# Kernel tuning notes

Measured on AMD Instinct MI355X. Metric: run time of the kernel, lower is better.

The kernel has to match this reference:

```python
import jax, jax.numpy as jnp
import numpy as np

COMMITMENT_COST = 0.25
NUM_EMBEDDINGS = 512
EMBEDDING_DIM = 128


def setup_inputs() -> dict:
    key = jax.random.key(0)
    k1, k2 = jax.random.split(key)
    z = jax.random.normal(k1, (64, 128, 32, 32), dtype=jnp.float32)
    # nn.Embedding weight initialized uniform(-1/K, 1/K)
    lim = 1.0 / NUM_EMBEDDINGS
    emb_weight = jax.random.uniform(
        k2, (NUM_EMBEDDINGS, EMBEDDING_DIM), dtype=jnp.float32,
        minval=-lim, maxval=lim)
    return {"z": z, "emb_weight": emb_weight}


def reference(z, emb_weight):
    b, c, h, w = z.shape  # c == embedding_dim
    # (b, h, w, c) -> (b*h*w, c)
    z_cl = jnp.transpose(z, (0, 2, 3, 1))
    z_flat = z_cl.reshape(b * h * w, c)
    # squared L2 distances: ||z||^2 + ||e||^2 - 2 z.e  -> [N, K]
    distances = (
        jnp.sum(z_flat ** 2, axis=-1, keepdims=True)
        + jnp.sum(emb_weight ** 2, axis=-1)[None, :]
        - 2.0 * jnp.matmul(z_flat, emb_weight.T)
    )
    encoding_indices = jnp.argmin(distances, axis=-1)  # [N]
    z_q = emb_weight[encoding_indices]                 # [N, c]
    z_q = z_q.reshape(b, h, w, c)
    z_q = jnp.transpose(z_q, (0, 3, 1, 2))             # [b, c, h, w]
    loss = (
        jnp.mean((z_q - jax.lax.stop_gradient(z)) ** 2)
        + COMMITMENT_COST * jnp.mean((jax.lax.stop_gradient(z_q) - z) ** 2)
    )
    # straight-through estimator
    z_q_st = z + jax.lax.stop_gradient(z_q - z)
    return (z_q_st, loss, encoding_indices)
```

## Files before the change

kernel.cpp:

```cpp
#include <hip/hip_runtime.h>


#define D_DIM 128
#define HW    1024
#define GAP_THR 2.5e-4f
#define FLAG_CAP 16384

typedef short short8 __attribute__((ext_vector_type(8)));
typedef float f32x16 __attribute__((ext_vector_type(16)));

union U8 { unsigned int u[4]; short8 s; uint4 q; };

__device__ __forceinline__ unsigned short f2bf(float v) {
    unsigned int u = __builtin_bit_cast(unsigned int, v);
    return (unsigned short)((u + 0x7fffu + ((u >> 16) & 1u)) >> 16);
}
__device__ __forceinline__ float bfhi(unsigned short h) {
    unsigned int u = ((unsigned int)h) << 16;
    return __builtin_bit_cast(float, u);
}
__device__ __forceinline__ unsigned int umn(unsigned int a, unsigned int b) {
    return a < b ? a : b;
}
__device__ __forceinline__ unsigned int umx(unsigned int a, unsigned int b) {
    return a > b ? a : b;
}

__global__ void prep_kernel(const float* __restrict__ emb,
                            float* __restrict__ etr,
                            uint4* __restrict__ ebh, uint4* __restrict__ ebl,
                            float* __restrict__ se) {
    const int t = blockIdx.x * 256 + threadIdx.x;

    {
        const int k = t >> 7;
        const int d = t & 127;
        etr[d * 512 + k] = emb[t];
    }

    if (t < 8192) {
        const int lane = t & 63;
        const int ks   = (t >> 6) & 7;
        const int kcol = t >> 9;
        const int krow = kcol * 32 + (lane & 31);
        const int d0   = ks * 16 + (lane >> 5) * 8;
        const float* ep = emb + (size_t)krow * D_DIM + d0;
        float v[8];
        #pragma unroll
        for (int j = 0; j < 8; ++j) v[j] = ep[j];
        U8 hh, ll;
        #pragma unroll
        for (int p = 0; p < 4; ++p) {
            const unsigned short h0 = f2bf(v[2*p]), h1 = f2bf(v[2*p+1]);
            const unsigned short l0 = f2bf(v[2*p]   - bfhi(h0));
            const unsigned short l1 = f2bf(v[2*p+1] - bfhi(h1));
            hh.u[p] = (unsigned int)h0 | ((unsigned int)h1 << 16);
            ll.u[p] = (unsigned int)l0 | ((unsigned int)l1 << 16);
        }
        ebh[t] = hh.q;
        ebl[t] = ll.q;
    }

    if (t < 512) {
        const float* e = emb + (size_t)t * D_DIM;
        float r[8];
        #pragma unroll
        for (int j = 0; j < 8; ++j) {
            float v = e[j];
            float p = v * v;
            asm("" : "+v"(p));
            r[j] = p;
        }
        for (int i = 8; i < 128; i += 8) {
            #pragma unroll
            for (int j = 0; j < 8; ++j) {
                float v = e[i + j];
                float p = v * v;
                asm("" : "+v"(p));
                r[j] += p;
            }
        }
        se[t] = ((r[0] + r[1]) + (r[2] + r[3])) + ((r[4] + r[5]) + (r[6] + r[7]));
    }
}

__launch_bounds__(256, 1)
__global__ void dist_kernel(const float* __restrict__ z,
                            const uint4* __restrict__ ebh,
                            const uint4* __restrict__ ebl,
                            const float* __restrict__ se_g,
                            const float* __restrict__ emb,
                            float* __restrict__ idx_out,
                            unsigned int* __restrict__ flag_cnt,
                            int* __restrict__ flag_list,
                            float* __restrict__ zq,
                            double* __restrict__ loss) {
    __shared__ int   li_sh[128];
    __shared__ float ept[D_DIM * 33];
    __shared__ float lred[4];

    const int tid  = threadIdx.x;
    const int lane = tid & 63;
    const int wid  = tid >> 6;
    const int row  = lane & 31;
    const int nblk = blockIdx.x * 128;
    const int bimg = nblk >> 10;
    const int hw0  = nblk & 1023;
    const int n0   = nblk + wid * 32;
    const int hww  = hw0 + wid * 32;

    short8 Ah[8], Al[8];
    {
        const float* zc = z + (size_t)bimg * (D_DIM * HW) + hww + row;
        #pragma unroll
        for (int ks = 0; ks < 8; ++ks) {
            const int d0 = ks * 16 + (lane >> 5) * 8;
            float v[8];
            #pragma unroll
            for (int j = 0; j < 8; ++j) v[j] = zc[(size_t)(d0 + j) * HW];
            U8 hh, ll;
            #pragma unroll
            for (int p = 0; p < 4; ++p) {
                unsigned int hwd, lwd;
                asm("v_cvt_pk_bf16_f32 %0, %1, %2" : "=v"(hwd) : "v"(v[2*p]), "v"(v[2*p+1]));
                const float xh = __builtin_bit_cast(float, hwd << 16);
                const float yh = __builtin_bit_cast(float, hwd & 0xffff0000u);
                const float xl = v[2*p]   - xh;
                const float yl = v[2*p+1] - yh;
                asm("v_cvt_pk_bf16_f32 %0, %1, %2" : "=v"(lwd) : "v"(xl), "v"(yl));
                hh.u[p] = hwd; ll.u[p] = lwd;
            }
            Ah[ks] = hh.s; Al[ks] = ll.s;
        }
    }

    unsigned int b1[16], b2[16];
    #pragma unroll
    for (int j = 0; j < 16; ++j) { b1[j] = 0xFFFFFFFFu; b2[j] = 0xFFFFFFFFu; }

    for (int kc = 0; kc < 16; ++kc) {
        const int   kgl  = kc * 32 + row;
        const float sevp = se_g[kgl] + 0.5f;
        const uint4* pbh = ebh + kc * 512 + lane;
        const uint4* pbl = ebl + kc * 512 + lane;

        f32x16 ahh, ahl, alh;
        #pragma unroll
        for (int j = 0; j < 16; ++j) { ahh[j] = 0.f; ahl[j] = 0.f; alh[j] = 0.f; }

        #pragma unroll
        for (int ks = 0; ks < 8; ++ks) {
            U8 bh; bh.q = pbh[ks * 64];
            U8 bl; bl.q = pbl[ks * 64];
            ahh = __builtin_amdgcn_mfma_f32_32x32x16_bf16(Ah[ks], bh.s, ahh, 0, 0, 0);
            ahl = __builtin_amdgcn_mfma_f32_32x32x16_bf16(Ah[ks], bl.s, ahl, 0, 0, 0);
            alh = __builtin_amdgcn_mfma_f32_32x32x16_bf16(Al[ks], bh.s, alh, 0, 0, 0);
        }

        #pragma unroll
        for (int j = 0; j < 16; ++j) {
            const float dot = (ahh[j] + ahl[j]) + alh[j];
            const float pd  = fmaf(-2.f, dot, sevp);
            const unsigned int key =
                (__builtin_bit_cast(unsigned int, pd) & 0xFFFFFE00u) | (unsigned int)kgl;
            const unsigned int m = umn(key, b1[j]);
            b2[j] = umn(umx(key, b1[j]), b2[j]);
            b1[j] = m;
        }
    }

    #pragma unroll
    for (int off = 1; off <= 16; off <<= 1) {
        #pragma unroll
        for (int j = 0; j < 16; ++j) {
            const unsigned int o1 = (unsigned int)__shfl_xor((int)b1[j], off);
            const unsigned int o2 = (unsigned int)__shfl_xor((int)b2[j], off);
            const unsigned int m  = umn(b1[j], o1);
            b2[j] = umn(umx(b1[j], o1), umn(b2[j], o2));
            b1[j] = m;
        }
    }

    if ((lane & 31) == 0) {
        const int half = lane >> 5;
        #pragma unroll
        for (int j = 0; j < 16; ++j) {
            const int r = (j & 3) + 8 * (j >> 2) + 4 * half;
            const int n = n0 + r;
            const int code = (int)(b1[j] & 511u);
            idx_out[n] = (float)code;
            li_sh[wid * 32 + r] = code;
            const float f1 = __builtin_bit_cast(float, b1[j] & 0xFFFFFE00u);
            const float f2 = __builtin_bit_cast(float, b2[j] & 0xFFFFFE00u);
            if (f2 - f1 < GAP_THR) {
                unsigned int p = atomicAdd(flag_cnt, 1u);
                if (p < FLAG_CAP) flag_list[p] = n;
            }
        }
    }

    float lacc = 0.f;
    for (int h = 0; h < 4; ++h) {
        __syncthreads();
        {
            const int p   = tid >> 3;
            const int sub = tid & 7;
            const float* er = emb + (size_t)li_sh[h * 32 + p] * D_DIM + sub * 16;
            #pragma unroll
            for (int j4 = 0; j4 < 4; ++j4) {
                const float4 v = *(const float4*)(er + j4 * 4);
                const int c = sub * 16 + j4 * 4;
                ept[(c + 0) * 33 + p] = v.x;
                ept[(c + 1) * 33 + p] = v.y;
                ept[(c + 2) * 33 + p] = v.z;
                ept[(c + 3) * 33 + p] = v.w;
            }
        }
        __syncthreads();
        {
            const int p  = tid & 31;
            const int c0 = tid >> 5;
            const int hwp = hw0 + h * 32 + p;
            const float* zb2 = z  + (size_t)bimg * (D_DIM * HW) + hwp;
            float*       qb  = zq + (size_t)bimg * (D_DIM * HW) + hwp;
            #pragma unroll
            for (int i = 0; i < 16; ++i) {
                const int c = c0 + i * 8;
                const float v  = ept[c * 33 + p];
                const float zv = zb2[(size_t)c * HW];
                qb[(size_t)c * HW] = v;
                const float df = v - zv;
                lacc = fmaf(df, df, lacc);
            }
        }
    }
    #pragma unroll
    for (int off = 32; off > 0; off >>= 1) lacc += __shfl_down(lacc, off);
    if (lane == 0) lred[wid] = lacc;
    __syncthreads();
    if (tid == 0)
        atomicAdd(loss, (double)(lred[0] + lred[1] + lred[2] + lred[3]));
}

__launch_bounds__(512)
__global__ void fixup_kernel(const float* __restrict__ z,
                             const float* __restrict__ etr,
                             const unsigned int* __restrict__ flag_cnt,
                             const int* __restrict__ flag_list,
                             const float* __restrict__ se_np,
                             float* __restrict__ idx_out) {
    __shared__ float zrow[D_DIM];
    __shared__ float q[D_DIM];
    __shared__ float rsum[8];
    __shared__ float szs;
    __shared__ float rv[8];
    __shared__ int   rix[8];

    const int tid = threadIdx.x;
    unsigned int cnt = *flag_cnt;
    if (cnt > FLAG_CAP) cnt = FLAG_CAP;

    for (unsigned int f = blockIdx.x; f < cnt; f += gridDim.x) {
        const int row = flag_list[f];
        const int b   = row >> 10;
        const int hw  = row & 1023;
        __syncthreads();
        if (tid < D_DIM) {
            float v = z[(size_t)b * (D_DIM * HW) + (size_t)tid * HW + hw];
            zrow[tid] = v;
            q[tid] = v * v;
        }
        __syncthreads();
        if (tid < 8) {
            float r = q[tid];
            for (int i = 8; i < 128; i += 8) r += q[i + tid];
            rsum[tid] = r;
        }
        __syncthreads();
        if (tid == 0)
            szs = ((rsum[0] + rsum[1]) + (rsum[2] + rsum[3]))
                + ((rsum[4] + rsum[5]) + (rsum[6] + rsum[7]));
        __syncthreads();
        const float sz32 = szs;

        const int k = tid;
        double dot0 = 0.0, dot1 = 0.0;
        #pragma unroll 4
        for (int d = 0; d < D_DIM; d += 2) {
            dot0 += (double)etr[d * 512 + k]       * (double)zrow[d];
            dot1 += (double)etr[(d + 1) * 512 + k] * (double)zrow[d + 1];
        }
        const float dotf = (float)(dot0 + dot1);
        const float T    = sz32 + se_np[k];
        float best  = T - 2.0f * dotf;
        int   besti = k;

        #pragma unroll
        for (int off = 32; off > 0; off >>= 1) {
            const float ov = __shfl_down(best, off);
            const int   oi = __shfl_down(besti, off);
            if (ov < best || (ov == best && oi < besti)) { best = ov; besti = oi; }
        }
        if ((tid & 63) == 0) { rv[tid >> 6] = best; rix[tid >> 6] = besti; }
        __syncthreads();
        if (tid == 0) {
            #pragma unroll
            for (int w = 1; w < 8; ++w)
                if (rv[w] < best || (rv[w] == best && rix[w] < besti)) {
                    best = rv[w]; besti = rix[w];
                }
            idx_out[row] = (float)besti;
        }
    }
}

__global__ void fin_kernel(const double* __restrict__ loss, float* __restrict__ out_loss) {
    *out_loss = (float)(*loss * 1.25 / 8388608.0);
}

extern "C" void kernel_launch(void* const* d_in, const int* in_sizes, int n_in,
                              void* d_out, int out_size, void* d_ws, size_t ws_size,
                              hipStream_t stream) {
    const float* z   = (const float*)d_in[0];
    const float* emb = (const float*)d_in[1];
    float* out      = (float*)d_out;
    float* zq       = out;
    float* out_loss = out + 8388608;
    float* idx_f    = out + 8388609;

    char* ws = (char*)d_ws;
    unsigned int* flag_cnt = (unsigned int*)ws;
    double*       loss     = (double*)(ws + 8);
    float*        se       = (float*)(ws + 10240);
    uint4*        ebh      = (uint4*)(ws + 16384);
    uint4*        ebl      = (uint4*)(ws + 16384 + 131072);
    int*          flag_list= (int*)(ws + 16384 + 262144);
    float*        etr      = (float*)(ws + 16384 + 262144 + 65536);

    hipMemsetAsync(d_ws, 0, 16384, stream);
    prep_kernel <<<256,  256, 0, stream>>>(emb, etr, ebh, ebl, se);
    dist_kernel <<<512,  256, 0, stream>>>(z, ebh, ebl, se, emb, idx_f,
                                           flag_cnt, flag_list, zq, loss);
    fixup_kernel<<<2048, 512, 0, stream>>>(z, etr, flag_cnt, flag_list, se, idx_f);
    fin_kernel  <<<1,    1,   0, stream>>>(loss, out_loss);
}
```

Before: 111.0 us.

## Double-buffer codebook chunks in LDS via async global-to-LDS loads

After: 106.5 us. -4.1%, faster.

```diff
diff --git a/kernel.cpp b/kernel.cpp
--- a/kernel.cpp
+++ b/kernel.cpp
@@ -24,6 +24,11 @@
 }
 __device__ __forceinline__ unsigned int umx(unsigned int a, unsigned int b) {
     return a > b ? a : b;
+}
+__device__ __forceinline__ void gl_lds16(const void* g, void* l) {
+    __builtin_amdgcn_global_load_lds(
+        (const __attribute__((address_space(1))) unsigned int*)g,
+        (__attribute__((address_space(3))) unsigned int*)l, 16, 0, 0);
 }
 
 __global__ void prep_kernel(const float* __restrict__ emb,
@@ -95,6 +100,7 @@
                             int* __restrict__ flag_list,
                             float* __restrict__ zq,
                             double* __restrict__ loss) {
+    __shared__ unsigned int ebs[2][4096];
     __shared__ int   li_sh[128];
     __shared__ float ept[D_DIM * 33];
     __shared__ float lred[4];
@@ -138,11 +144,35 @@
     #pragma unroll
     for (int j = 0; j < 16; ++j) { b1[j] = 0xFFFFFFFFu; b2[j] = 0xFFFFFFFFu; }
 
+    {
+        const unsigned int* sh_ = (const unsigned int*)ebh;
+        const unsigned int* sl_ = (const unsigned int*)ebl;
+        #pragma unroll
+        for (int i = 0; i < 2; ++i) {
+            const int seg  = wid * 2 + i;
+            const int gofs = seg * 256 + lane * 4;
+            gl_lds16(sh_ + gofs, (char*)&ebs[0][0]    + seg * 1024);
+            gl_lds16(sl_ + gofs, (char*)&ebs[0][2048] + seg * 1024);
+        }
+    }
+    __syncthreads();
+
+    int buf = 0;
     for (int kc = 0; kc < 16; ++kc) {
+        if (kc < 15) {
+            const unsigned int* sh_ = (const unsigned int*)(ebh + (kc + 1) * 512);
+            const unsigned int* sl_ = (const unsigned int*)(ebl + (kc + 1) * 512);
+            #pragma unroll
+            for (int i = 0; i < 2; ++i) {
+                const int seg  = wid * 2 + i;
+                const int gofs = seg * 256 + lane * 4;
+                gl_lds16(sh_ + gofs, (char*)&ebs[buf ^ 1][0]    + seg * 1024);
+                gl_lds16(sl_ + gofs, (char*)&ebs[buf ^ 1][2048] + seg * 1024);
+            }
+        }
+
         const int   kgl  = kc * 32 + row;
         const float sevp = se_g[kgl] + 0.5f;
-        const uint4* pbh = ebh + kc * 512 + lane;
-        const uint4* pbl = ebl + kc * 512 + lane;
 
         f32x16 ahh, ahl, alh;
         #pragma unroll
@@ -150,11 +180,11 @@
 
         #pragma unroll
         for (int ks = 0; ks < 8; ++ks) {
-            U8 bh; bh.q = pbh[ks * 64];
-            U8 bl; bl.q = pbl[ks * 64];
-            ahh = __builtin_amdgcn_mfma_f32_32x32x16_bf16(Ah[ks], bh.s, ahh, 0, 0, 0);
-            ahl = __builtin_amdgcn_mfma_f32_32x32x16_bf16(Ah[ks], bl.s, ahl, 0, 0, 0);
-            alh = __builtin_amdgcn_mfma_f32_32x32x16_bf16(Al[ks], bh.s, alh, 0, 0, 0);
+            const short8 bh = *(const short8*)&ebs[buf][ks * 256 + lane * 4];
+            const short8 bl = *(const short8*)&ebs[buf][2048 + ks * 256 + lane * 4];
+            ahh = __builtin_amdgcn_mfma_f32_32x32x16_bf16(Ah[ks], bh, ahh, 0, 0, 0);
+            ahl = __builtin_amdgcn_mfma_f32_32x32x16_bf16(Ah[ks], bl, ahl, 0, 0, 0);
+            alh = __builtin_amdgcn_mfma_f32_32x32x16_bf16(Al[ks], bh, alh, 0, 0, 0);
         }
 
         #pragma unroll
@@ -167,6 +197,9 @@
             b2[j] = umn(umx(key, b1[j]), b2[j]);
             b1[j] = m;
         }
+
+        __syncthreads();
+        buf ^= 1;
     }
 
     #pragma unroll
```

## Split codebook search across wave pairs and double dist_kernel grid

Applied to the files above, without the earlier changes.

After: 101.1 us. 1.1x faster.

```diff
diff --git a/kernel.cpp b/kernel.cpp
--- a/kernel.cpp
+++ b/kernel.cpp
@@ -95,19 +95,21 @@
                             int* __restrict__ flag_list,
                             float* __restrict__ zq,
                             double* __restrict__ loss) {
-    __shared__ int   li_sh[128];
+    __shared__ unsigned int red1[2][64], red2[2][64];
+    __shared__ int   li_sh[64];
     __shared__ float ept[D_DIM * 33];
     __shared__ float lred[4];
 
     const int tid  = threadIdx.x;
     const int lane = tid & 63;
     const int wid  = tid >> 6;
+    const int wn   = wid >> 1;
+    const int wk   = wid & 1;
     const int row  = lane & 31;
-    const int nblk = blockIdx.x * 128;
+    const int nblk = blockIdx.x * 64;
     const int bimg = nblk >> 10;
     const int hw0  = nblk & 1023;
-    const int n0   = nblk + wid * 32;
-    const int hww  = hw0 + wid * 32;
+    const int hww  = hw0 + wn * 32;
 
     short8 Ah[8], Al[8];
     {
@@ -138,7 +140,8 @@
     #pragma unroll
     for (int j = 0; j < 16; ++j) { b1[j] = 0xFFFFFFFFu; b2[j] = 0xFFFFFFFFu; }
 
-    for (int kc = 0; kc < 16; ++kc) {
+    for (int i = 0; i < 8; ++i) {
+        const int   kc   = wk * 8 + i;
         const int   kgl  = kc * 32 + row;
         const float sevp = se_g[kgl] + 0.5f;
         const uint4* pbh = ebh + kc * 512 + lane;
@@ -185,22 +188,32 @@
         const int half = lane >> 5;
         #pragma unroll
         for (int j = 0; j < 16; ++j) {
-            const int r = (j & 3) + 8 * (j >> 2) + 4 * half;
-            const int n = n0 + r;
-            const int code = (int)(b1[j] & 511u);
-            idx_out[n] = (float)code;
-            li_sh[wid * 32 + r] = code;
-            const float f1 = __builtin_bit_cast(float, b1[j] & 0xFFFFFE00u);
-            const float f2 = __builtin_bit_cast(float, b2[j] & 0xFFFFFE00u);
-            if (f2 - f1 < GAP_THR) {
-                unsigned int p = atomicAdd(flag_cnt, 1u);
-                if (p < FLAG_CAP) flag_list[p] = n;
-            }
+            const int r = wn * 32 + (j & 3) + 8 * (j >> 2) + 4 * half;
+            red1[wk][r] = b1[j];
+            red2[wk][r] = b2[j];
+        }
+    }
+    __syncthreads();
+
+    if (tid < 64) {
+        const unsigned int v1a = red1[0][tid], v2a = red2[0][tid];
+        const unsigned int v1b = red1[1][tid], v2b = red2[1][tid];
+        const unsigned int m1 = umn(v1a, v1b);
+        const unsigned int m2 = umn(umn(v2a, v2b), umx(v1a, v1b));
+        const int n = nblk + tid;
+        const int code = (int)(m1 & 511u);
+        idx_out[n] = (float)code;
+        li_sh[tid] = code;
+        const float f1 = __builtin_bit_cast(float, m1 & 0xFFFFFE00u);
+        const float f2 = __builtin_bit_cast(float, m2 & 0xFFFFFE00u);
+        if (f2 - f1 < GAP_THR) {
+            unsigned int p = atomicAdd(flag_cnt, 1u);
+            if (p < FLAG_CAP) flag_list[p] = n;
         }
     }
 
     float lacc = 0.f;
-    for (int h = 0; h < 4; ++h) {
+    for (int h = 0; h < 2; ++h) {
         __syncthreads();
         {
             const int p   = tid >> 3;
@@ -339,7 +352,7 @@
 
     hipMemsetAsync(d_ws, 0, 16384, stream);
     prep_kernel <<<256,  256, 0, stream>>>(emb, etr, ebh, ebl, se);
-    dist_kernel <<<512,  256, 0, stream>>>(z, ebh, ebl, se, emb, idx_f,
+    dist_kernel <<<1024, 256, 0, stream>>>(z, ebh, ebl, se, emb, idx_f,
                                            flag_cnt, flag_list, zq, loss);
     fixup_kernel<<<2048, 512, 0, stream>>>(z, etr, flag_cnt, flag_list, se, idx_f);
     fin_kernel  <<<1,    1,   0, stream>>>(loss, out_loss);
```

## Switch distance GEMM to 16x16x32 MFMA with smaller blocks and higher occupancy

Applied to the files above, without the earlier changes.

New measurement: 112.6 us. No clear change (+1.5%).

```diff
diff --git a/kernel.cpp b/kernel.cpp
--- a/kernel.cpp
+++ b/kernel.cpp
@@ -7,7 +7,7 @@
 #define FLAG_CAP 16384
 
 typedef short short8 __attribute__((ext_vector_type(8)));
-typedef float f32x16 __attribute__((ext_vector_type(16)));
+typedef float f32x4 __attribute__((ext_vector_type(4)));
 
 union U8 { unsigned int u[4]; short8 s; uint4 q; };
 
@@ -40,10 +40,10 @@
 
     if (t < 8192) {
         const int lane = t & 63;
-        const int ks   = (t >> 6) & 7;
-        const int kcol = t >> 9;
-        const int krow = kcol * 32 + (lane & 31);
-        const int d0   = ks * 16 + (lane >> 5) * 8;
+        const int ks   = (t >> 6) & 3;
+        const int kcol = t >> 8;
+        const int krow = kcol * 16 + (lane & 15);
+        const int d0   = ks * 32 + (lane >> 4) * 8;
         const float* ep = emb + (size_t)krow * D_DIM + d0;
         float v[8];
         #pragma unroll
@@ -84,7 +84,7 @@
     }
 }
 
-__launch_bounds__(256, 1)
+__launch_bounds__(256, 4)
 __global__ void dist_kernel(const float* __restrict__ z,
                             const uint4* __restrict__ ebh,
                             const uint4* __restrict__ ebl,
@@ -95,26 +95,29 @@
                             int* __restrict__ flag_list,
                             float* __restrict__ zq,
                             double* __restrict__ loss) {
-    __shared__ int   li_sh[128];
+    __shared__ int   li_sh[64];
     __shared__ float ept[D_DIM * 33];
     __shared__ float lred[4];
 
-    const int tid  = threadIdx.x;
-    const int lane = tid & 63;
-    const int wid  = tid >> 6;
-    const int row  = lane & 31;
-    const int nblk = blockIdx.x * 128;
+    const int tid   = threadIdx.x;
+    const int lane  = tid & 63;
+    const int wid   = tid >> 6;
+    const int row16 = lane & 15;
+    const int kgrp  = lane >> 4;
+    const int bidl = (int)blockIdx.x;
+    const int bid  = (bidl & 7) * 128 + (bidl >> 3);
+    const int nblk = bid * 64;
     const int bimg = nblk >> 10;
     const int hw0  = nblk & 1023;
-    const int n0   = nblk + wid * 32;
-    const int hww  = hw0 + wid * 32;
-
-    short8 Ah[8], Al[8];
+    const int n0   = nblk + wid * 16;
+    const int hww  = hw0 + wid * 16;
+
+    short8 Ah[4], Al[4];
     {
-        const float* zc = z + (size_t)bimg * (D_DIM * HW) + hww + row;
-        #pragma unroll
-        for (int ks = 0; ks < 8; ++ks) {
-            const int d0 = ks * 16 + (lane >> 5) * 8;
+        const float* zc = z + (size_t)bimg * (D_DIM * HW) + hww + row16;
+        #pragma unroll
+        for (int ks = 0; ks < 4; ++ks) {
+            const int d0 = ks * 32 + kgrp * 8;
             float v[8];
             #pragma unroll
             for (int j = 0; j < 8; ++j) v[j] = zc[(size_t)(d0 + j) * HW];
@@ -134,35 +137,38 @@
         }
     }
 
-    unsigned int b1[16], b2[16];
+    unsigned int b1[4], b2[4];
     #pragma unroll
-    for (int j = 0; j < 16; ++j) { b1[j] = 0xFFFFFFFFu; b2[j] = 0xFFFFFFFFu; }
-
-    for (int kc = 0; kc < 16; ++kc) {
-        const int   kgl  = kc * 32 + row;
-        const float sevp = se_g[kgl] + 0.5f;
-        const uint4* pbh = ebh + kc * 512 + lane;
-        const uint4* pbl = ebl + kc * 512 + lane;
-
-        f32x16 ahh, ahl, alh;
-        #pragma unroll
-        for (int j = 0; j < 16; ++j) { ahh[j] = 0.f; ahl[j] = 0.f; alh[j] = 0.f; }
-
-        #pragma unroll
-        for (int ks = 0; ks < 8; ++ks) {
+    for (int j = 0; j < 4; ++j) { b1[j] = 0xFFFFFFFFu; b2[j] = 0xFFFFFFFFu; }
+
+    for (int col = 0; col < 32; ++col) {
+        const int   code = col * 16 + row16;
+        const float sevp = se_g[code] + 0.5f;
+        const uint4* pbh = ebh + col * 256 + lane;
+        const uint4* pbl = ebl + col * 256 + lane;
+
+        f32x4 chh, chl, clh;
+        #pragma unroll
+        for (int j = 0; j < 4; ++j) { chh[j] = 0.f; chl[j] = 0.f; clh[j] = 0.f; }
+
+        __builtin_amdgcn_s_setprio(1);
+        #pragma unroll
+        for (int ks = 0; ks < 4; ++ks) {
             U8 bh; bh.q = pbh[ks * 64];
             U8 bl; bl.q = pbl[ks * 64];
-            ahh = __builtin_amdgcn_mfma_f32_32x32x16_bf16(Ah[ks], bh.s, ahh, 0, 0, 0);
-            ahl = __builtin_amdgcn_mfma_f32_32x32x16_bf16(Ah[ks], bl.s, ahl, 0, 0, 0);
-            alh = __builtin_amdgcn_mfma_f32_32x32x16_bf16(Al[ks], bh.s, alh, 0, 0, 0);
-        }
-
-        #pragma unroll
-        for (int j = 0; j < 16; ++j) {
-            const float dot = (ahh[j] + ahl[j]) + alh[j];
-            const float pd  = fmaf(-2.f, dot, sevp);
+            chh = __builtin_amdgcn_mfma_f32_16x16x32_bf16(Ah[ks], bh.s, chh, 0, 0, 0);
+            chl = __builtin_amdgcn_mfma_f32_16x16x32_bf16(Ah[ks], bl.s, chl, 0, 0, 0);
+            clh = __builtin_amdgcn_mfma_f32_16x16x32_bf16(Al[ks], bh.s, clh, 0, 0, 0);
+        }
+        __builtin_amdgcn_s_setprio(0);
+
+        #pragma unroll
+        for (int j = 0; j < 4; ++j) {
+            const float pd = fmaf(-2.f, chh[j],
+                             fmaf(-2.f, chl[j],
+                             fmaf(-2.f, clh[j], sevp)));
             const unsigned int key =
-                (__builtin_bit_cast(unsigned int, pd) & 0xFFFFFE00u) | (unsigned int)kgl;
+                (__builtin_bit_cast(unsigned int, pd) & 0xFFFFFE00u) | (unsigned int)code;
             const unsigned int m = umn(key, b1[j]);
             b2[j] = umn(umx(key, b1[j]), b2[j]);
             b1[j] = m;
@@ -170,9 +176,9 @@
     }
 
     #pragma unroll
-    for (int off = 1; off <= 16; off <<= 1) {
-        #pragma unroll
-        for (int j = 0; j < 16; ++j) {
+    for (int off = 1; off <= 8; off <<= 1) {
+        #pragma unroll
+        for (int j = 0; j < 4; ++j) {
             const unsigned int o1 = (unsigned int)__shfl_xor((int)b1[j], off);
             const unsigned int o2 = (unsigned int)__shfl_xor((int)b2[j], off);
             const unsigned int m  = umn(b1[j], o1);
@@ -181,15 +187,14 @@
         }
     }
 
-    if ((lane & 31) == 0) {
-        const int half = lane >> 5;
-        #pragma unroll
-        for (int j = 0; j < 16; ++j) {
-            const int r = (j & 3) + 8 * (j >> 2) + 4 * half;
+    if (row16 == 0) {
+        #pragma unroll
+        for (int j = 0; j < 4; ++j) {
+            const int r = kgrp * 4 + j;
             const int n = n0 + r;
             const int code = (int)(b1[j] & 511u);
             idx_out[n] = (float)code;
-            li_sh[wid * 32 + r] = code;
+            li_sh[wid * 16 + r] = code;
             const float f1 = __builtin_bit_cast(float, b1[j] & 0xFFFFFE00u);
             const float f2 = __builtin_bit_cast(float, b2[j] & 0xFFFFFE00u);
             if (f2 - f1 < GAP_THR) {
@@ -200,7 +205,7 @@
     }
 
     float lacc = 0.f;
-    for (int h = 0; h < 4; ++h) {
+    for (int h = 0; h < 2; ++h) {
         __syncthreads();
         {
             const int p   = tid >> 3;
@@ -339,7 +344,7 @@
 
     hipMemsetAsync(d_ws, 0, 16384, stream);
     prep_kernel <<<256,  256, 0, stream>>>(emb, etr, ebh, ebl, se);
-    dist_kernel <<<512,  256, 0, stream>>>(z, ebh, ebl, se, emb, idx_f,
+    dist_kernel <<<1024, 256, 0, stream>>>(z, ebh, ebl, se, emb, idx_f,
                                            flag_cnt, flag_list, zq, loss);
     fixup_kernel<<<2048, 512, 0, stream>>>(z, etr, flag_cnt, flag_list, se, idx_f);
     fin_kernel  <<<1,    1,   0, stream>>>(loss, out_loss);
```
